# Kernel optimization log

Measured on AMD Instinct MI355X. Metric: run time of the kernel, lower is better.

The kernel has to match this reference:

```python
import jax, jax.numpy as jnp
import numpy as np

T, N, C, S = 512, 32, 5000, 100
BLANK = 0
NEG = -1e30  # log-space 'zero'


def setup_inputs() -> dict:
    key = jax.random.key(0)
    k1, k2, k3 = jax.random.split(key, 3)
    logits = jax.random.normal(k1, (T, N, C), dtype=jnp.float32)
    log_probs = jax.nn.log_softmax(logits, axis=-1)  # CTC expects log-probs
    targets = jax.random.randint(k2, (N, S), 1, C)   # labels never equal blank(=0)
    input_lengths = jnp.full((N,), T, dtype=jnp.int32)
    target_lengths = jax.random.randint(k3, (N,), S // 2, S + 1).astype(jnp.int32)
    return {"log_probs": log_probs, "targets": targets,
            "input_lengths": input_lengths, "target_lengths": target_lengths}


def _logsumexp3(a, b, c):
    m = jnp.maximum(jnp.maximum(a, b), c)
    return m + jnp.log(jnp.exp(a - m) + jnp.exp(b - m) + jnp.exp(c - m))


def _ctc_loss(log_probs, targets, input_lengths, target_lengths, blank=BLANK):
    Tm, Nb, Cc = log_probs.shape
    Sm = targets.shape[1]
    L = 2 * Sm + 1  # extended (blank-interleaved) label lattice width

    # extended targets: [blank, t0, blank, t1, ..., blank]  -> shape [N, L]
    ext = jnp.full((Nb, L), blank, dtype=targets.dtype)
    ext = ext.at[:, 1::2].set(targets)
    is_label = (jnp.arange(L) % 2 == 1)
    ext_prev2 = jnp.concatenate(
        [jnp.full((Nb, 2), -1, dtype=ext.dtype), ext[:, :-2]], axis=1)
    allow_skip = is_label[None, :] & (ext != ext_prev2)          # [N, L]
    pos_mask = jnp.arange(L)[None, :] < (2 * target_lengths + 1)[:, None]

    def emit(lp_t):  # lp_t: [N, C] -> [N, L] gather of label log-probs
        return jnp.take_along_axis(lp_t, ext, axis=1)

    # init alpha at t=0
    e0 = emit(log_probs[0])
    alpha0 = jnp.full((Nb, L), NEG, dtype=log_probs.dtype)
    alpha0 = alpha0.at[:, 0].set(e0[:, 0])
    alpha0 = alpha0.at[:, 1].set(jnp.where(target_lengths > 0, e0[:, 1], NEG))
    alpha0 = jnp.where(pos_mask, alpha0, NEG)

    neg1 = jnp.full((Nb, 1), NEG, dtype=log_probs.dtype)
    neg2 = jnp.full((Nb, 2), NEG, dtype=log_probs.dtype)

    def step(alpha, xs):
        lp_t, t = xs
        a1 = jnp.concatenate([neg1, alpha[:, :-1]], axis=1)
        a2 = jnp.where(allow_skip,
                       jnp.concatenate([neg2, alpha[:, :-2]], axis=1), NEG)
        new = _logsumexp3(alpha, a1, a2) + emit(lp_t)
        new = jnp.where(pos_mask, new, NEG)
        active = (t < input_lengths)[:, None]  # freeze alpha past input length
        return jnp.where(active, new, alpha), None

    alpha, _ = jax.lax.scan(step, alpha0,
                            (log_probs[1:], jnp.arange(1, Tm)))

    # total log-likelihood: last blank + last label states
    last = (2 * target_lengths).astype(jnp.int32)
    a_blank = jnp.take_along_axis(alpha, last[:, None], axis=1)[:, 0]
    a_label = jnp.take_along_axis(alpha, jnp.maximum(last - 1, 0)[:, None], axis=1)[:, 0]
    m = jnp.maximum(a_blank, a_label)
    ll = m + jnp.log(jnp.exp(a_blank - m) + jnp.exp(a_label - m))
    loss = -ll
    # zero_infinity=True: zero out infinite losses
    loss = jnp.where(jnp.isfinite(loss) & (loss < 1e29), loss, 0.0)
    # reduction='mean': divide by target_lengths (clamped to 1), then batch mean
    loss = loss / jnp.maximum(target_lengths, 1).astype(loss.dtype)
    return jnp.mean(loss)


def reference(log_probs, targets, input_lengths, target_lengths):
    return _ctc_loss(log_probs, targets, input_lengths, target_lengths)
```

## Files before the change

kernel.cpp:

```cpp
#include <hip/hip_runtime.h>
#include <cstdint>
#include <cmath>

#define Tt   512
#define Nb   32
#define Cc   5000
#define Sm   100
#define Lw   201
#define Lpad 256
#define NEGV (-1e30f)
#define TCH  8

__device__ __forceinline__ float lse2(float a, float b) {
    float m = fmaxf(a, b);
    return m + __logf(1.0f + __expf(fminf(a, b) - m));
}
__device__ __forceinline__ float lse3(float a, float b, float c) {
    float m   = fmaxf(fmaxf(a, b), c);
    float mid = __builtin_amdgcn_fmed3f(a, b, c);
    float lo  = fminf(fminf(a, b), c);
    return m + __logf(1.0f + __expf(mid - m) + __expf(lo - m));
}

__global__ __launch_bounds__(256, 1)
void ctc_gather_kernel(const float* __restrict__ lp,
                       const int*   __restrict__ tgt,
                       const int*   __restrict__ tlen,
                       float*       __restrict__ em)
{
    const int bid = blockIdx.x;
    const int n   = bid >> 6;
    const int t0  = (bid & 63) * TCH;
    const int l   = threadIdx.x;

    const int Lact = 2 * tlen[n] + 1;

    int e = 0;
    if (l & 1) {
        int j = (l - 1) >> 1;
        if (j < Sm) e = tgt[n * Sm + j];
    }
    const bool live = (l < Lact);

    const float* src = lp + (size_t)n * Cc + e;
    float v[TCH];
#pragma unroll
    for (int k = 0; k < TCH; ++k)
        v[k] = live ? src[(size_t)(t0 + k) * (Nb * Cc)] : NEGV;

    float* dst = em + (((size_t)n * Tt + t0) << 8) + l;
#pragma unroll
    for (int k = 0; k < TCH; ++k)
        dst[k << 8] = v[k];
}

__global__ __launch_bounds__(64, 1)
void ctc_alpha_wave_kernel(const float* __restrict__ em,
                           const int*   __restrict__ tgt,
                           const int*   __restrict__ ilen,
                           const int*   __restrict__ tlen,
                           float*       __restrict__ per_loss)
{
    const int n = blockIdx.x;
    const int i = threadIdx.x;

    const int tl = tlen[n];
    const int il = ilen[n];

    const int j1 = 2 * i, j3 = 2 * i + 1;
    bool s1 = false, s3 = false;
    if (j1 >= 1 && j1 < Sm) s1 = (tgt[n * Sm + j1] != tgt[n * Sm + j1 - 1]);
    if (j3 >= 1 && j3 < Sm) s3 = (tgt[n * Sm + j3] != tgt[n * Sm + j3 - 1]);

    const float4* emv = (const float4*)em + ((size_t)n << 15);

    float4 E0 = emv[i];
    float a0 = (i == 0)           ? E0.x : NEGV;
    float a1 = (i == 0 && tl > 0) ? E0.y : NEGV;
    float a2 = NEGV;
    float a3 = NEGV;

    constexpr int PF = 16;
    float4 ebuf[PF];
#pragma unroll
    for (int k = 0; k < PF; ++k) {
        int t = 1 + k;
        ebuf[k] = (t < Tt) ? emv[(t << 6) + i]
                           : make_float4(NEGV, NEGV, NEGV, NEGV);
    }

    for (int tb = 1; tb < Tt; tb += PF) {
#pragma unroll
        for (int k = 0; k < PF; ++k) {
            const int t = tb + k;
            if (t < Tt) {
                float4 e  = ebuf[k];
                int    tp = t + PF;
                if (tp < Tt) ebuf[k] = emv[(tp << 6) + i];

                float p3  = __shfl_up(a3, 1);
                float am0 = (i > 0) ? p3 : NEGV;

                float n0 = lse2(a0, am0)                + e.x;
                float n1 = lse3(a1, a0, s1 ? p3 : NEGV) + e.y;
                float n2 = lse2(a2, a1)                 + e.z;
                float n3 = lse3(a3, a2, s3 ? a1 : NEGV) + e.w;

                if (t < il) {
                    a0 = n0; a1 = n1; a2 = n2; a3 = n3;
                }
            }
        }
    }

    const int lb = 2 * tl;
    const int lv = (lb - 1 >= 0) ? lb - 1 : 0;

    int   cb = lb & 3;
    float vb = (cb == 0) ? a0 : (cb == 1) ? a1 : (cb == 2) ? a2 : a3;
    float ab = __shfl(vb, lb >> 2);
    int   cl = lv & 3;
    float vl = (cl == 0) ? a0 : (cl == 1) ? a1 : (cl == 2) ? a2 : a3;
    float al = __shfl(vl, lv >> 2);

    if (i == 0) {
        float m    = fmaxf(ab, al);
        float ll   = m + __logf(__expf(ab - m) + __expf(al - m));
        float loss = -ll;
        if (!(isfinite(loss) && loss < 1e29f)) loss = 0.0f;
        int   d    = (tl >= 1) ? tl : 1;
        per_loss[n] = loss / (float)d;
    }
}

__global__ void ctc_finalize_kernel(const float* __restrict__ per_loss,
                                    float* __restrict__ out)
{
    int i = threadIdx.x;
    float v = (i < Nb) ? per_loss[i] : 0.0f;
#pragma unroll
    for (int off = 32; off > 0; off >>= 1)
        v += __shfl_down(v, off, 64);
    if (i == 0) out[0] = v * (1.0f / Nb);
}

extern "C" void kernel_launch(void* const* d_in, const int* in_sizes, int n_in,
                              void* d_out, int out_size, void* d_ws, size_t ws_size,
                              hipStream_t stream)
{
    const float* lp   = (const float*)d_in[0];
    const int*   tgt  = (const int*)  d_in[1];
    const int*   ilen = (const int*)  d_in[2];
    const int*   tlen = (const int*)  d_in[3];
    float*       out  = (float*)d_out;

    float* per_loss = (float*)d_ws;
    float* em       = (float*)((char*)d_ws + 256);

    ctc_gather_kernel<<<Nb * (Tt / TCH), 256, 0, stream>>>(lp, tgt, tlen, em);
    ctc_alpha_wave_kernel<<<Nb, 64, 0, stream>>>(em, tgt, ilen, tlen, per_loss);
    ctc_finalize_kernel<<<1, 64, 0, stream>>>(per_loss, out);
}
```

Before: 522.1 us.

## Compact emission layout, separate blank stream, and compute alpha in base-2 log space

Result: faster. 491.9 us (-5.8%).

```diff
diff --git a/kernel.cpp b/kernel.cpp
--- a/kernel.cpp
+++ b/kernel.cpp
@@ -6,56 +6,71 @@
 #define Nb   32
 #define Cc   5000
 #define Sm   100
-#define Lw   201
-#define Lpad 256
 #define NEGV (-1e30f)
+#define LOG2E 1.4426950408889634f
+#define LN2   0.6931471805599453f
 #define TCH  8
 
-__device__ __forceinline__ float lse2(float a, float b) {
+#if __has_builtin(__builtin_amdgcn_exp2f)
+#define EXP2F(x) __builtin_amdgcn_exp2f(x)
+#else
+#define EXP2F(x) exp2f(x)
+#endif
+#if __has_builtin(__builtin_amdgcn_logf)
+#define LOG2F(x) __builtin_amdgcn_logf(x)
+#else
+#define LOG2F(x) log2f(x)
+#endif
+
+__device__ __forceinline__ float lse2_l2(float a, float b) {
     float m = fmaxf(a, b);
-    return m + __logf(1.0f + __expf(fminf(a, b) - m));
+    return m + LOG2F(1.0f + EXP2F(fminf(a, b) - m));
 }
-__device__ __forceinline__ float lse3(float a, float b, float c) {
+__device__ __forceinline__ float lse3_l2(float a, float b, float c) {
     float m   = fmaxf(fmaxf(a, b), c);
     float mid = __builtin_amdgcn_fmed3f(a, b, c);
     float lo  = fminf(fminf(a, b), c);
-    return m + __logf(1.0f + __expf(mid - m) + __expf(lo - m));
+    return m + LOG2F(1.0f + EXP2F(mid - m) + EXP2F(lo - m));
 }
 
-__global__ __launch_bounds__(256, 1)
+__global__ __launch_bounds__(128, 1)
 void ctc_gather_kernel(const float* __restrict__ lp,
                        const int*   __restrict__ tgt,
-                       const int*   __restrict__ tlen,
-                       float*       __restrict__ em)
+                       float*       __restrict__ em2,
+                       float*       __restrict__ bl)
 {
     const int bid = blockIdx.x;
     const int n   = bid >> 6;
     const int t0  = (bid & 63) * TCH;
-    const int l   = threadIdx.x;
+    const int j   = threadIdx.x;
 
-    const int Lact = 2 * tlen[n] + 1;
+    float* dst = em2 + (((size_t)n * Tt + t0) << 7) + j;
 
-    int e = 0;
-    if (l & 1) {
-        int j = (l - 1) >> 1;
-        if (j < Sm) e = tgt[n * Sm + j];
+    if (j < Sm) {
+        const int e = tgt[n * Sm + j];
+        const float* src = lp + (size_t)n * Cc + e;
+        float v[TCH];
+#pragma unroll
+        for (int k = 0; k < TCH; ++k)
+            v[k] = src[(size_t)(t0 + k) * (Nb * Cc)];
+#pragma unroll
+        for (int k = 0; k < TCH; ++k)
+            dst[k << 7] = v[k] * LOG2E;
+    } else {
+#pragma unroll
+        for (int k = 0; k < TCH; ++k)
+            dst[k << 7] = NEGV;
+        if (j < Sm + TCH) {
+            int k = j - Sm;
+            bl[n * Tt + t0 + k] =
+                lp[(size_t)(t0 + k) * (Nb * Cc) + (size_t)n * Cc] * LOG2E;
+        }
     }
-    const bool live = (l < Lact);
-
-    const float* src = lp + (size_t)n * Cc + e;
-    float v[TCH];
-#pragma unroll
-    for (int k = 0; k < TCH; ++k)
-        v[k] = live ? src[(size_t)(t0 + k) * (Nb * Cc)] : NEGV;
-
-    float* dst = em + (((size_t)n * Tt + t0) << 8) + l;
-#pragma unroll
-    for (int k = 0; k < TCH; ++k)
-        dst[k << 8] = v[k];
 }
 
 __global__ __launch_bounds__(64, 1)
-void ctc_alpha_wave_kernel(const float* __restrict__ em,
+void ctc_alpha_wave_kernel(const float* __restrict__ em2,
+                           const float* __restrict__ bl,
                            const int*   __restrict__ tgt,
                            const int*   __restrict__ ilen,
                            const int*   __restrict__ tlen,
@@ -70,23 +85,25 @@
     const int j1 = 2 * i, j3 = 2 * i + 1;
     bool s1 = false, s3 = false;
     if (j1 >= 1 && j1 < Sm) s1 = (tgt[n * Sm + j1] != tgt[n * Sm + j1 - 1]);
-    if (j3 >= 1 && j3 < Sm) s3 = (tgt[n * Sm + j3] != tgt[n * Sm + j3 - 1]);
+    if (j3 < Sm)            s3 = (tgt[n * Sm + j3] != tgt[n * Sm + j3 - 1]);
 
-    const float4* emv = (const float4*)em + ((size_t)n << 15);
+    const float2* e2 = (const float2*)em2 + ((size_t)n << 15);
+    const float*  bn = bl + n * Tt;
 
-    float4 E0 = emv[i];
-    float a0 = (i == 0)           ? E0.x : NEGV;
-    float a1 = (i == 0 && tl > 0) ? E0.y : NEGV;
+    const int pull = (i > 0 ? i - 1 : 0) << 2;
+
+    float2 E0 = e2[i];
+    float a0 = (i == 0)           ? bn[0] : NEGV;
+    float a1 = (i == 0 && tl > 0) ? E0.x  : NEGV;
     float a2 = NEGV;
     float a3 = NEGV;
 
-    constexpr int PF = 16;
-    float4 ebuf[PF];
+    constexpr int PF = 8;
+    float2 ebuf[PF];
 #pragma unroll
     for (int k = 0; k < PF; ++k) {
         int t = 1 + k;
-        ebuf[k] = (t < Tt) ? emv[(t << 6) + i]
-                           : make_float4(NEGV, NEGV, NEGV, NEGV);
+        ebuf[k] = (t < Tt) ? e2[(t << 6) + i] : make_float2(NEGV, NEGV);
     }
 
     for (int tb = 1; tb < Tt; tb += PF) {
@@ -94,17 +111,19 @@
         for (int k = 0; k < PF; ++k) {
             const int t = tb + k;
             if (t < Tt) {
-                float4 e  = ebuf[k];
+                float2 e  = ebuf[k];
+                float  eb = bn[t];
                 int    tp = t + PF;
-                if (tp < Tt) ebuf[k] = emv[(tp << 6) + i];
+                if (tp < Tt) ebuf[k] = e2[(tp << 6) + i];
 
-                float p3  = __shfl_up(a3, 1);
+                float p3  = __int_as_float(
+                    __builtin_amdgcn_ds_bpermute(pull, __float_as_int(a3)));
                 float am0 = (i > 0) ? p3 : NEGV;
 
-                float n0 = lse2(a0, am0)                + e.x;
-                float n1 = lse3(a1, a0, s1 ? p3 : NEGV) + e.y;
-                float n2 = lse2(a2, a1)                 + e.z;
-                float n3 = lse3(a3, a2, s3 ? a1 : NEGV) + e.w;
+                float n0 = lse2_l2(a0, am0)                   + eb;
+                float n1 = lse3_l2(a1, a0, s1 ? p3 : NEGV)    + e.x;
+                float n2 = lse2_l2(a2, a1)                    + eb;
+                float n3 = lse3_l2(a3, a2, s3 ? a1 : NEGV)    + e.y;
 
                 if (t < il) {
                     a0 = n0; a1 = n1; a2 = n2; a3 = n3;
@@ -125,8 +144,8 @@
 
     if (i == 0) {
         float m    = fmaxf(ab, al);
-        float ll   = m + __logf(__expf(ab - m) + __expf(al - m));
-        float loss = -ll;
+        float ll2  = m + LOG2F(EXP2F(ab - m) + EXP2F(al - m));
+        float loss = -ll2 * LN2;
         if (!(isfinite(loss) && loss < 1e29f)) loss = 0.0f;
         int   d    = (tl >= 1) ? tl : 1;
         per_loss[n] = loss / (float)d;
@@ -155,9 +174,10 @@
     float*       out  = (float*)d_out;
 
     float* per_loss = (float*)d_ws;
-    float* em       = (float*)((char*)d_ws + 256);
+    float* bl       = (float*)((char*)d_ws + 256);
+    float* em2      = (float*)((char*)d_ws + 256 + (size_t)Nb * Tt * 4);
 
-    ctc_gather_kernel<<<Nb * (Tt / TCH), 256, 0, stream>>>(lp, tgt, tlen, em);
-    ctc_alpha_wave_kernel<<<Nb, 64, 0, stream>>>(em, tgt, ilen, tlen, per_loss);
+    ctc_gather_kernel<<<Nb * (Tt / TCH), 128, 0, stream>>>(lp, tgt, em2, bl);
+    ctc_alpha_wave_kernel<<<Nb, 64, 0, stream>>>(em2, bl, tgt, ilen, tlen, per_loss);
     ctc_finalize_kernel<<<1, 64, 0, stream>>>(per_loss, out);
 }
```
